# Kernel optimization log

Measured on AMD Instinct MI355X. Metric: run time of the kernel, lower is better.

## Reference

```python
import jax, jax.numpy as jnp
import numpy as np

B, T, E, D, OUT = 2048, 64, 256, 256, 2


def setup_inputs() -> dict:
    key = jax.random.key(0)
    ks = jax.random.split(key, 16)
    s = 0.05
    return {
        "input_encoded": jax.random.normal(ks[0], (B, T, E), dtype=jnp.float32),
        "y_history": jax.random.normal(ks[1], (B, T), dtype=jnp.float32),
        # attn_layer: Linear(2D+E -> E), Tanh, Linear(E -> 1)
        "W1": jax.random.normal(ks[2], (E, 2 * D + E), dtype=jnp.float32) * s,
        "b1": jax.random.normal(ks[3], (E,), dtype=jnp.float32) * s,
        "w2": jax.random.normal(ks[4], (E,), dtype=jnp.float32) * s,
        "b2": jax.random.normal(ks[5], (1,), dtype=jnp.float32) * s,
        # single-layer LSTM(input=OUT, hidden=D); gate order i,f,g,o
        "W_ih": jax.random.normal(ks[6], (4 * D, OUT), dtype=jnp.float32) * s,
        "b_ih": jax.random.normal(ks[7], (4 * D,), dtype=jnp.float32) * s,
        "W_hh": jax.random.normal(ks[8], (4 * D, D), dtype=jnp.float32) * s,
        "b_hh": jax.random.normal(ks[9], (4 * D,), dtype=jnp.float32) * s,
        # fc: Linear(E+T -> OUT) (torch init normal_() std=1; scaled here for stability)
        "W_fc": jax.random.normal(ks[10], (OUT, E + T), dtype=jnp.float32) * s,
        "b_fc": jax.random.normal(ks[11], (OUT,), dtype=jnp.float32) * s,
        # fc_final: Linear(D+E -> OUT)
        "W_final": jax.random.normal(ks[12], (OUT, D + E), dtype=jnp.float32) * s,
        "b_final": jax.random.normal(ks[13], (OUT,), dtype=jnp.float32) * s,
    }


def reference(input_encoded, y_history, W1, b1, w2, b2, W_ih, b_ih, W_hh, b_hh,
              W_fc, b_fc, W_final, b_final):
    Bs, Ts, Es = input_encoded.shape
    Ds = W_hh.shape[1]

    def step(carry, _):
        h, c, _ctx = carry  # h, c: [B, D]
        hc = jnp.concatenate([h, c], axis=-1)  # [B, 2D]
        hc_rep = jnp.broadcast_to(hc[:, None, :], (Bs, Ts, 2 * Ds))
        x = jnp.concatenate([hc_rep, input_encoded], axis=-1)  # [B, T, 2D+E]
        scores = jnp.tanh(x @ W1.T + b1) @ w2 + b2  # [B, T]
        alpha = jax.nn.softmax(scores, axis=1)
        ctx = jnp.einsum('bt,bte->be', alpha, input_encoded)  # [B, E]
        y_tilde = jnp.concatenate([ctx, y_history], axis=1) @ W_fc.T + b_fc  # [B, OUT]
        gates = y_tilde @ W_ih.T + b_ih + h @ W_hh.T + b_hh  # [B, 4D]
        i, f, g, o = jnp.split(gates, 4, axis=-1)
        c_new = jax.nn.sigmoid(f) * c + jax.nn.sigmoid(i) * jnp.tanh(g)
        h_new = jax.nn.sigmoid(o) * jnp.tanh(c_new)
        return (h_new, c_new, ctx), None

    init = (jnp.zeros((Bs, Ds), input_encoded.dtype),
            jnp.zeros((Bs, Ds), input_encoded.dtype),
            jnp.zeros((Bs, Es), input_encoded.dtype))
    (h, c, ctx), _ = jax.lax.scan(step, init, None, length=Ts)
    return jnp.concatenate([h, ctx], axis=1) @ W_final.T + b_final  # [B, OUT]
```

## Files before the change

kernel.cpp:

```cpp
#include <hip/hip_runtime.h>
#include <hip/hip_bf16.h>
#include <cstdint>
#include <cstddef>

#define LOG2E 1.44269504088896340736f

using f32x4 = __attribute__((ext_vector_type(4))) float;
using s16x8 = __attribute__((ext_vector_type(8))) short;

static __device__ __forceinline__ float bf2f(unsigned short u) {
  union { unsigned int i; float f; } v; v.i = ((unsigned int)u) << 16; return v.f;
}
static __device__ __forceinline__ unsigned short f2bf(float f) {
  union { float f; unsigned int i; } v; v.f = f;
  unsigned int r = v.i + 0x7fffu + ((v.i >> 16) & 1u);
  return (unsigned short)(r >> 16);
}
static __device__ __forceinline__ float wredmax(float v) {
  #pragma unroll
  for (int m = 32; m > 0; m >>= 1) v = fmaxf(v, __shfl_xor(v, m, 64));
  return v;
}
static __device__ __forceinline__ float wredsum(float v) {
  #pragma unroll
  for (int m = 32; m > 0; m >>= 1) v += __shfl_xor(v, m, 64);
  return v;
}

__global__ void ktrans(const float* __restrict__ W1, const float* __restrict__ b1,
                       const float* __restrict__ Wih_in, const float* __restrict__ bih,
                       const float* __restrict__ Whh, const float* __restrict__ bhh,
                       const float* __restrict__ Wfc, const float* __restrict__ bfc,
                       const float* __restrict__ yhist,
                       unsigned short* __restrict__ WB1, unsigned short* __restrict__ WBhh,
                       unsigned short* __restrict__ WB1e, float* __restrict__ b1s,
                       float* __restrict__ Wihs, float* __restrict__ gbias,
                       float* __restrict__ yh2)
{
  int idx = blockIdx.x * 256 + threadIdx.x;
  const float TS = 2.f * LOG2E;
  if (idx < 131072) {
    int k = idx >> 8, e = idx & 255;
    WB1[((k >> 3) * 256 + e) * 8 + (k & 7)] = f2bf(TS * W1[e * 768 + k]);
    return;
  }
  idx -= 131072;
  if (idx < 262144) {
    int k = idx >> 10, j = idx & 1023;
    float sc = ((j >> 8) == 2) ? TS : -LOG2E;
    WBhh[((k >> 3) * 1024 + j) * 8 + (k & 7)] = f2bf(sc * Whh[j * 256 + k]);
    return;
  }
  idx -= 262144;
  if (idx < 65536) {
    int k = idx >> 8, e = idx & 255;
    WB1e[((k >> 3) * 256 + e) * 8 + (k & 7)] = f2bf(TS * W1[e * 768 + 512 + k]);
    return;
  }
  idx -= 65536;
  if (idx < 256) { b1s[idx] = TS * b1[idx]; return; }
  idx -= 256;
  if (idx < 2048) {
    int j = idx >> 1;
    float sc = ((j >> 8) == 2) ? TS : -LOG2E;
    Wihs[idx] = sc * Wih_in[idx];
    return;
  }
  idx -= 2048;
  if (idx < 1024) {
    int j = idx;
    float sc = ((j >> 8) == 2) ? TS : -LOG2E;
    gbias[j] = sc * (bih[j] + bhh[j]);
    return;
  }
  idx -= 1024;
  if (idx < 4096) {
    int bq = idx >> 1, o = idx & 1;
    float a = bfc[o];
    for (int t = 0; t < 64; ++t) a = fmaf(yhist[bq * 64 + t], Wfc[o * 320 + 256 + t], a);
    yh2[idx] = a;
    return;
  }
}

__global__ __launch_bounds__(256, 4) void kpre(
    const float* __restrict__ x, const unsigned short* __restrict__ WB1e,
    const float* __restrict__ Wfc,
    unsigned short* __restrict__ P, float* __restrict__ ey)
{
  __shared__ __align__(16) unsigned short xs[16384];
  const int bq = blockIdx.x;
  const int tid = threadIdx.x;
  const int w = tid >> 6, lane = tid & 63;
  const float* __restrict__ xb = x + (size_t)bq * 16384;

  #pragma unroll 4
  for (int it = 0; it < 16; ++it) {
    int idx = it * 256 + tid;
    float4 v = *(const float4*)(xb + (size_t)idx * 4);
    int t = idx >> 6, e0 = (idx & 63) * 4;
    unsigned long long pk = (unsigned long long)f2bf(v.x)
        | ((unsigned long long)f2bf(v.y) << 16)
        | ((unsigned long long)f2bf(v.z) << 32)
        | ((unsigned long long)f2bf(v.w) << 48);
    int ba = (t * 512 + e0 * 2) ^ ((t & 7) << 4);
    *(unsigned long long*)((char*)xs + ba) = pk;
  }
  __syncthreads();

  const int mt = w;
  const int fgrp = lane >> 4, fcol = lane & 15;
  const int trow = mt * 16 + fcol;
  s16x8 af[8];
  #pragma unroll
  for (int kb = 0; kb < 8; ++kb) {
    int e = kb * 32 + fgrp * 8;
    int ba = (trow * 512 + e * 2) ^ ((trow & 7) << 4);
    af[kb] = *(const s16x8*)((char*)xs + ba);
  }
  __syncthreads();

  unsigned short* __restrict__ Pst = xs;
  #pragma unroll
  for (int nt = 0; nt < 16; ++nt) {
    s16x8 bfr[8];
    #pragma unroll
    for (int kb = 0; kb < 8; ++kb)
      bfr[kb] = *(const s16x8*)&WB1e[(size_t)((kb * 4 + fgrp) * 256 + nt * 16 + fcol) * 8];
    f32x4 acc = {0.f, 0.f, 0.f, 0.f};
    #pragma unroll
    for (int kb = 0; kb < 8; ++kb)
      acc = __builtin_amdgcn_mfma_f32_16x16x32_bf16(af[kb], bfr[kb], acc, 0, 0, 0);
    const int ep = nt * 16 + fcol;
    #pragma unroll
    for (int r = 0; r < 4; ++r)
      Pst[(mt * 16 + fgrp * 4 + r) * 256 + ep] = f2bf(acc[r]);
  }
  __syncthreads();

  unsigned int* __restrict__ Pd = (unsigned int*)(P + (size_t)bq * 16384);
  #pragma unroll 4
  for (int d = tid; d < 8192; d += 256) {
    int f = d * 2;
    int ec = f >> 9, t = (f >> 3) & 63, i0 = f & 7;
    unsigned int lo = Pst[t * 256 + ec * 8 + i0];
    unsigned int hi = Pst[t * 256 + ec * 8 + i0 + 1];
    Pd[d] = lo | (hi << 16);
  }

  if (tid < 128) {
    int t = tid >> 1, o = tid & 1;
    float a = 0.f;
    const float* __restrict__ xr = xb + t * 256;
    const float* __restrict__ wr = Wfc + o * 320;
    #pragma unroll 4
    for (int e = 0; e < 256; ++e) a = fmaf(xr[e], wr[e], a);
    ey[((size_t)bq * 64 + t) * 2 + o] = a;
  }
}

#define SIG(X) __builtin_amdgcn_rcpf(1.f + __builtin_amdgcn_exp2f(X))

#define SCCHUNK(PV, EC) do { \
  const float4 qa_ = *(const float4*)(qrow + (EC) * 8); \
  const float4 qc_ = *(const float4*)(qrow + (EC) * 8 + 4); \
  const float4 wa_ = *(const float4*)(w2f + (EC) * 8); \
  const float4 wc_ = *(const float4*)(w2f + (EC) * 8 + 4); \
  a0 = fmaf(wa_.x, SIG(bf2f((unsigned short)(PV)[0]) + qa_.x), a0); \
  a1 = fmaf(wa_.y, SIG(bf2f((unsigned short)(PV)[1]) + qa_.y), a1); \
  a2 = fmaf(wa_.z, SIG(bf2f((unsigned short)(PV)[2]) + qa_.z), a2); \
  a3 = fmaf(wa_.w, SIG(bf2f((unsigned short)(PV)[3]) + qa_.w), a3); \
  a0 = fmaf(wc_.x, SIG(bf2f((unsigned short)(PV)[4]) + qc_.x), a0); \
  a1 = fmaf(wc_.y, SIG(bf2f((unsigned short)(PV)[5]) + qc_.y), a1); \
  a2 = fmaf(wc_.z, SIG(bf2f((unsigned short)(PV)[6]) + qc_.z), a2); \
  a3 = fmaf(wc_.w, SIG(bf2f((unsigned short)(PV)[7]) + qc_.w), a3); \
} while (0)

#define SCL(EC) do { \
  const s16x8 pvL_ = *(const s16x8*)&Plds[b][(EC) - 16][lane][0]; \
  SCCHUNK(pvL_, EC); \
} while (0)

#define AH(KB) (*(const s16x8*)&hcA[(((KB) * 4 + fgrp) * 8 + frow) * 8])

#define GUNIT(U, S0, S1, S2, S3) do { \
  const size_t jb_ = (size_t)((((U) & 3) * 256 + ((U) >> 2) * 128 + w * 16 + fcol)) * 8; \
  const s16x8 wb0_ = *(const s16x8*)&WBhh[jb_ + (size_t)(0 * 4 + fgrp) * 8192]; \
  const s16x8 wb1_ = *(const s16x8*)&WBhh[jb_ + (size_t)(1 * 4 + fgrp) * 8192]; \
  const s16x8 wb2_ = *(const s16x8*)&WBhh[jb_ + (size_t)(2 * 4 + fgrp) * 8192]; \
  const s16x8 wb3_ = *(const s16x8*)&WBhh[jb_ + (size_t)(3 * 4 + fgrp) * 8192]; \
  const s16x8 wb4_ = *(const s16x8*)&WBhh[jb_ + (size_t)(4 * 4 + fgrp) * 8192]; \
  const s16x8 wb5_ = *(const s16x8*)&WBhh[jb_ + (size_t)(5 * 4 + fgrp) * 8192]; \
  const s16x8 wb6_ = *(const s16x8*)&WBhh[jb_ + (size_t)(6 * 4 + fgrp) * 8192]; \
  const s16x8 wb7_ = *(const s16x8*)&WBhh[jb_ + (size_t)(7 * 4 + fgrp) * 8192]; \
  G##U = (f32x4){gb_##U, gb_##U, gb_##U, gb_##U}; \
  S0; S1; S2; S3; \
  G##U = __builtin_amdgcn_mfma_f32_16x16x32_bf16(AH(0), wb0_, G##U, 0, 0, 0); \
  G##U = __builtin_amdgcn_mfma_f32_16x16x32_bf16(AH(1), wb1_, G##U, 0, 0, 0); \
  G##U = __builtin_amdgcn_mfma_f32_16x16x32_bf16(AH(2), wb2_, G##U, 0, 0, 0); \
  G##U = __builtin_amdgcn_mfma_f32_16x16x32_bf16(AH(3), wb3_, G##U, 0, 0, 0); \
  G##U = __builtin_amdgcn_mfma_f32_16x16x32_bf16(AH(4), wb4_, G##U, 0, 0, 0); \
  G##U = __builtin_amdgcn_mfma_f32_16x16x32_bf16(AH(5), wb5_, G##U, 0, 0, 0); \
  G##U = __builtin_amdgcn_mfma_f32_16x16x32_bf16(AH(6), wb6_, G##U, 0, 0, 0); \
  G##U = __builtin_amdgcn_mfma_f32_16x16x32_bf16(AH(7), wb7_, G##U, 0, 0, 0); \
} while (0)

#define PW(CG, R, CV, Gi, Gf, Gg, Go, w0i, w1i, w0f, w1f, w0g, w1g, w0o, w1o) do { \
  const int row_ = (drow0 + (R)) & 7; \
  const int jj_ = (CG) * 128 + w * 16 + fcol; \
  const float y0_ = yt[row_][0], y1_ = yt[row_][1]; \
  const float gi_ = (Gi)[R] + fmaf(w0i, y0_, (w1i) * y1_); \
  const float gf_ = (Gf)[R] + fmaf(w0f, y0_, (w1f) * y1_); \
  const float gg_ = (Gg)[R] + fmaf(w0g, y0_, (w1g) * y1_); \
  const float go_ = (Go)[R] + fmaf(w0o, y0_, (w1o) * y1_); \
  const float si_ = SIG(gi_); \
  const float sf_ = SIG(gf_); \
  const float tg_ = 1.f - 2.f * SIG(gg_); \
  const float so_ = SIG(go_); \
  const float cn_ = sf_ * (CV) + si_ * tg_; \
  (CV) = cn_; \
  const float th_ = 1.f - 2.f * SIG(2.f * LOG2E * cn_); \
  const float hn_ = so_ * th_; \
  if (lane < 32) { \
    hcA[((jj_ >> 3) * 8 + row_) * 8 + (jj_ & 7)] = f2bf(hn_); \
    hcA[((32 + (jj_ >> 3)) * 8 + row_) * 8 + (jj_ & 7)] = f2bf(cn_); \
    if (s == 63) qf[row_][jj_] = hn_; \
  } \
} while (0)

#define PLOADR(U) const s16x8 p##U = *(const s16x8*)(Pb + (size_t)((U) * 64 + lane) * 8);

#define WIGB(U) \
  const int j##U = (((U) & 3) * 256 + ((U) >> 2) * 128 + w * 16 + fcol); \
  const float wi0_##U = Wihs[2 * j##U]; \
  const float wi1_##U = Wihs[2 * j##U + 1]; \
  const float gb_##U = gbias[j##U];

__global__
__attribute__((amdgpu_flat_work_group_size(512, 512), amdgpu_waves_per_eu(1, 2)))
void krecur(
    const float* __restrict__ x, const float* __restrict__ w2g,
    const unsigned short* __restrict__ WB1, const unsigned short* __restrict__ WBhh,
    const float* __restrict__ Wihs, const float* __restrict__ gbias,
    const float* __restrict__ b1s, const float* __restrict__ yh2,
    const float* __restrict__ ey, const unsigned short* __restrict__ P,
    const float* __restrict__ Wfin, const float* __restrict__ bfin,
    float* __restrict__ out)
{
  __shared__ __align__(16) unsigned short Plds[8][16][64][8];
  __shared__ __align__(16) unsigned short hcA[4096];
  __shared__ __align__(16) float qf[8][256];
  __shared__ __align__(16) float w2f[256];
  __shared__ __align__(16) float scAl[8][64];
  __shared__ float yt[8][2];

  const int tid = threadIdx.x;
  const int w = tid >> 6, lane = tid & 63;
  const int b = w;
  const int gbase = blockIdx.x * 8;
  const int gb = gbase + b;

  for (int i = tid; i < 4096; i += 512) hcA[i] = 0;
  if (tid < 256) w2f[tid] = w2g[tid];
  for (int i = tid; i < 8192; i += 512) {
    int row = i >> 10, rem = i & 1023, ec = rem >> 6, t = rem & 63;
    *(s16x8*)&Plds[row][ec][t][0] =
        *(const s16x8*)(P + (size_t)(gbase + row) * 16384 + (size_t)((16 + ec) * 64 + t) * 8);
  }

  const int frow = lane & 7;
  const int fgrp = lane >> 4;
  const int fcol = lane & 15;
  const int drow0 = fgrp * 4;

  const unsigned short* __restrict__ Pb = P + (size_t)gb * 16384;
  PLOADR(0)  PLOADR(1)  PLOADR(2)  PLOADR(3)
  PLOADR(4)  PLOADR(5)  PLOADR(6)  PLOADR(7)
  PLOADR(8)  PLOADR(9)  PLOADR(10) PLOADR(11)
  PLOADR(12) PLOADR(13) PLOADR(14) PLOADR(15)

  const float2 eyv = *(const float2*)(ey + ((size_t)gb * 64 + lane) * 2);
  const float yh0 = yh2[gb * 2], yh1 = yh2[gb * 2 + 1];
  const float b1r0 = b1s[(w * 2 + 0) * 16 + fcol];
  const float b1r1 = b1s[(w * 2 + 1) * 16 + fcol];

  WIGB(0) WIGB(1) WIGB(2) WIGB(3) WIGB(4) WIGB(5) WIGB(6) WIGB(7)

  float c0 = 0.f, c1 = 0.f, c2 = 0.f, c3 = 0.f;
  float c4 = 0.f, c5 = 0.f, c6 = 0.f, c7 = 0.f;

  __syncthreads();

  for (int s = 0; s < 64; ++s) {
    #pragma unroll
    for (int et2 = 0; et2 < 2; ++et2) {
      const int eb = (w * 2 + et2) * 16;
      f32x4 acc = {0.f, 0.f, 0.f, 0.f};
      #pragma unroll
      for (int kb = 0; kb < 16; ++kb) {
        const s16x8 bfr = *(const s16x8*)&WB1[(size_t)((kb * 4 + fgrp) * 256 + eb + fcol) * 8];
        acc = __builtin_amdgcn_mfma_f32_16x16x32_bf16(AH(kb), bfr, acc, 0, 0, 0);
      }
      if (lane < 32) {
        const float bb = et2 ? b1r1 : b1r0;
        #pragma unroll
        for (int r = 0; r < 4; ++r) qf[drow0 + r][eb + fcol] = acc[r] + bb;
      }
    }
    __syncthreads();

    float a0 = 0.f, a1 = 0.f, a2 = 0.f, a3 = 0.f;
    f32x4 G0, G1, G2, G3, G4, G5, G6, G7;
    const float* __restrict__ qrow = &qf[b][0];
    GUNIT(0, SCCHUNK(p0, 0),  SCCHUNK(p1, 1),  SCCHUNK(p2, 2),  SCCHUNK(p3, 3));
    GUNIT(1, SCCHUNK(p4, 4),  SCCHUNK(p5, 5),  SCCHUNK(p6, 6),  SCCHUNK(p7, 7));
    GUNIT(2, SCCHUNK(p8, 8),  SCCHUNK(p9, 9),  SCCHUNK(p10, 10), SCCHUNK(p11, 11));
    GUNIT(3, SCCHUNK(p12, 12), SCCHUNK(p13, 13), SCCHUNK(p14, 14), SCCHUNK(p15, 15));
    GUNIT(4, SCL(16), SCL(17), SCL(18), SCL(19));
    GUNIT(5, SCL(20), SCL(21), SCL(22), SCL(23));
    GUNIT(6, SCL(24), SCL(25), SCL(26), SCL(27));
    GUNIT(7, SCL(28), SCL(29), SCL(30), SCL(31));

    {
      float sc = -2.f * ((a0 + a1) + (a2 + a3));
      float mx = wredmax(sc);
      float e_t = __builtin_amdgcn_exp2f((sc - mx) * LOG2E);
      float sm = wredsum(e_t);
      float alpha = e_t * __builtin_amdgcn_rcpf(sm);
      if (s == 63) scAl[b][lane] = alpha;
      float y0 = wredsum(alpha * eyv.x);
      float y1 = wredsum(alpha * eyv.y);
      if (lane == 0) { yt[b][0] = y0 + yh0; yt[b][1] = y1 + yh1; }
    }
    __syncthreads();

    PW(0, 0, c0, G0, G1, G2, G3, wi0_0, wi1_0, wi0_1, wi1_1, wi0_2, wi1_2, wi0_3, wi1_3);
    PW(0, 1, c1, G0, G1, G2, G3, wi0_0, wi1_0, wi0_1, wi1_1, wi0_2, wi1_2, wi0_3, wi1_3);
    PW(0, 2, c2, G0, G1, G2, G3, wi0_0, wi1_0, wi0_1, wi1_1, wi0_2, wi1_2, wi0_3, wi1_3);
    PW(0, 3, c3, G0, G1, G2, G3, wi0_0, wi1_0, wi0_1, wi1_1, wi0_2, wi1_2, wi0_3, wi1_3);
    PW(1, 0, c4, G4, G5, G6, G7, wi0_4, wi1_4, wi0_5, wi1_5, wi0_6, wi1_6, wi0_7, wi1_7);
    PW(1, 1, c5, G4, G5, G6, G7, wi0_4, wi1_4, wi0_5, wi1_5, wi0_6, wi1_6, wi0_7, wi1_7);
    PW(1, 2, c6, G4, G5, G6, G7, wi0_4, wi1_4, wi0_5, wi1_5, wi0_6, wi1_6, wi0_7, wi1_7);
    PW(1, 3, c7, G4, G5, G6, G7, wi0_4, wi1_4, wi0_5, wi1_5, wi0_6, wi1_6, wi0_7, wi1_7);
    __syncthreads();

    if (s == 63) {
      float* __restrict__ ctxS = (float*)Plds;
      #pragma unroll
      for (int p = 0; p < 4; ++p) {
        const int e = p * 64 + lane;
        float a = 0.f;
        const float* __restrict__ xr = x + (size_t)gb * 16384 + e;
        #pragma unroll 8
        for (int t = 0; t < 64; ++t) a = fmaf(scAl[b][t], xr[t * 256], a);
        ctxS[b * 256 + e] = a;
      }
      __syncthreads();
    }
  }

  {
    const float* __restrict__ ctxS = (const float*)Plds;
    float o0 = 0.f, o1 = 0.f;
    #pragma unroll
    for (int kk = 0; kk < 8; ++kk) {
      const int k = kk * 64 + lane;
      const float v = (k < 256) ? qf[b][k] : ctxS[b * 256 + (k - 256)];
      o0 = fmaf(v, Wfin[k], o0);
      o1 = fmaf(v, Wfin[512 + k], o1);
    }
    o0 = wredsum(o0);
    o1 = wredsum(o1);
    if (lane == 0) {
      out[gb * 2 + 0] = o0 + bfin[0];
      out[gb * 2 + 1] = o1 + bfin[1];
    }
  }
}

extern "C" void kernel_launch(void* const* d_in, const int* in_sizes, int n_in,
                              void* d_out, int out_size, void* d_ws, size_t ws_size,
                              hipStream_t stream) {
  const float* x    = (const float*)d_in[0];
  const float* yh   = (const float*)d_in[1];
  const float* W1   = (const float*)d_in[2];
  const float* b1   = (const float*)d_in[3];
  const float* w2   = (const float*)d_in[4];
  const float* Wih  = (const float*)d_in[6];
  const float* bih  = (const float*)d_in[7];
  const float* Whh  = (const float*)d_in[8];
  const float* bhh  = (const float*)d_in[9];
  const float* Wfc  = (const float*)d_in[10];
  const float* bfc  = (const float*)d_in[11];
  const float* Wfin = (const float*)d_in[12];
  const float* bfin = (const float*)d_in[13];

  char* ws = (char*)d_ws;
  unsigned short* P    = (unsigned short*)(ws + 0);
  unsigned short* WB1  = (unsigned short*)(ws + 67108864);
  unsigned short* WBhh = (unsigned short*)(ws + 67371008);
  unsigned short* WB1e = (unsigned short*)(ws + 67895296);
  float* b1s   = (float*)(ws + 68026368);
  float* Wihs  = (float*)(ws + 68027392);
  float* gbias = (float*)(ws + 68035584);
  float* yh2   = (float*)(ws + 68039680);
  float* ey    = (float*)(ws + 68056064);

  ktrans<<<1821, 256, 0, stream>>>(W1, b1, Wih, bih, Whh, bhh, Wfc, bfc, yh,
                                   WB1, WBhh, WB1e, b1s, Wihs, gbias, yh2);
  kpre<<<2048, 256, 0, stream>>>(x, WB1e, Wfc, P, ey);
  krecur<<<256, 512, 0, stream>>>(x, w2, WB1, WBhh, Wihs, gbias, b1s, yh2, ey, P,
                                  Wfin, bfin, (float*)d_out);
}
```

Before: 4.068 ms.

## Double recurrence block to 1024 threads, splitting score and gate work per wave

The recurrent kernel now runs 16 waves per block instead of 8. Each batch row's attention score is split across two waves, and each wave handles half of the gate units. The LDS-resident half of the precomputed projection is dropped because every wave now holds its whole half in registers. Input-weight and gate-bias vectors move to shared memory, and an extra barrier plus a partial-score exchange buffer are added each step to combine the two halves. This trades more barrier traffic and tighter register budgets (waves_per_eu 4) for more parallel waves per compute unit and shorter per-wave serial work.

```diff
diff --git a/kernel.cpp b/kernel.cpp
--- a/kernel.cpp
+++ b/kernel.cpp
@@ -161,11 +161,11 @@
 
 #define SIG(X) __builtin_amdgcn_rcpf(1.f + __builtin_amdgcn_exp2f(X))
 
-#define SCCHUNK(PV, EC) do { \
-  const float4 qa_ = *(const float4*)(qrow + (EC) * 8); \
-  const float4 qc_ = *(const float4*)(qrow + (EC) * 8 + 4); \
-  const float4 wa_ = *(const float4*)(w2f + (EC) * 8); \
-  const float4 wc_ = *(const float4*)(w2f + (EC) * 8 + 4); \
+#define SCCHUNK(PV, U) do { \
+  const float4 qa_ = *(const float4*)(qrowh + (U) * 8); \
+  const float4 qc_ = *(const float4*)(qrowh + (U) * 8 + 4); \
+  const float4 wa_ = *(const float4*)(w2h + (U) * 8); \
+  const float4 wc_ = *(const float4*)(w2h + (U) * 8 + 4); \
   a0 = fmaf(wa_.x, SIG(bf2f((unsigned short)(PV)[0]) + qa_.x), a0); \
   a1 = fmaf(wa_.y, SIG(bf2f((unsigned short)(PV)[1]) + qa_.y), a1); \
   a2 = fmaf(wa_.z, SIG(bf2f((unsigned short)(PV)[2]) + qa_.z), a2); \
@@ -176,15 +176,11 @@
   a3 = fmaf(wc_.w, SIG(bf2f((unsigned short)(PV)[7]) + qc_.w), a3); \
 } while (0)
 
-#define SCL(EC) do { \
-  const s16x8 pvL_ = *(const s16x8*)&Plds[b][(EC) - 16][lane][0]; \
-  SCCHUNK(pvL_, EC); \
-} while (0)
-
-#define AH(KB) (*(const s16x8*)&hcA[(((KB) * 4 + fgrp) * 8 + frow) * 8])
-
-#define GUNIT(U, S0, S1, S2, S3) do { \
-  const size_t jb_ = (size_t)((((U) & 3) * 256 + ((U) >> 2) * 128 + w * 16 + fcol)) * 8; \
+#define AHF(KB) (*(const s16x8*)&hcA[(((KB) * 4 + fgrp) * 8 + frow) * 8])
+
+#define GUNIT4(GG) do { \
+  const int jg_ = (GG) * 256 + wv * 16 + fcol; \
+  const size_t jb_ = (size_t)jg_ * 8; \
   const s16x8 wb0_ = *(const s16x8*)&WBhh[jb_ + (size_t)(0 * 4 + fgrp) * 8192]; \
   const s16x8 wb1_ = *(const s16x8*)&WBhh[jb_ + (size_t)(1 * 4 + fgrp) * 8192]; \
   const s16x8 wb2_ = *(const s16x8*)&WBhh[jb_ + (size_t)(2 * 4 + fgrp) * 8192]; \
@@ -193,26 +189,25 @@
   const s16x8 wb5_ = *(const s16x8*)&WBhh[jb_ + (size_t)(5 * 4 + fgrp) * 8192]; \
   const s16x8 wb6_ = *(const s16x8*)&WBhh[jb_ + (size_t)(6 * 4 + fgrp) * 8192]; \
   const s16x8 wb7_ = *(const s16x8*)&WBhh[jb_ + (size_t)(7 * 4 + fgrp) * 8192]; \
-  G##U = (f32x4){gb_##U, gb_##U, gb_##U, gb_##U}; \
-  S0; S1; S2; S3; \
-  G##U = __builtin_amdgcn_mfma_f32_16x16x32_bf16(AH(0), wb0_, G##U, 0, 0, 0); \
-  G##U = __builtin_amdgcn_mfma_f32_16x16x32_bf16(AH(1), wb1_, G##U, 0, 0, 0); \
-  G##U = __builtin_amdgcn_mfma_f32_16x16x32_bf16(AH(2), wb2_, G##U, 0, 0, 0); \
-  G##U = __builtin_amdgcn_mfma_f32_16x16x32_bf16(AH(3), wb3_, G##U, 0, 0, 0); \
-  G##U = __builtin_amdgcn_mfma_f32_16x16x32_bf16(AH(4), wb4_, G##U, 0, 0, 0); \
-  G##U = __builtin_amdgcn_mfma_f32_16x16x32_bf16(AH(5), wb5_, G##U, 0, 0, 0); \
-  G##U = __builtin_amdgcn_mfma_f32_16x16x32_bf16(AH(6), wb6_, G##U, 0, 0, 0); \
-  G##U = __builtin_amdgcn_mfma_f32_16x16x32_bf16(AH(7), wb7_, G##U, 0, 0, 0); \
+  const float gbj_ = gbS[jg_]; \
+  GA##GG = (f32x4){gbj_, gbj_, gbj_, gbj_}; \
+  GA##GG = __builtin_amdgcn_mfma_f32_16x16x32_bf16(AHF(0), wb0_, GA##GG, 0, 0, 0); \
+  GA##GG = __builtin_amdgcn_mfma_f32_16x16x32_bf16(AHF(1), wb1_, GA##GG, 0, 0, 0); \
+  GA##GG = __builtin_amdgcn_mfma_f32_16x16x32_bf16(AHF(2), wb2_, GA##GG, 0, 0, 0); \
+  GA##GG = __builtin_amdgcn_mfma_f32_16x16x32_bf16(AHF(3), wb3_, GA##GG, 0, 0, 0); \
+  GA##GG = __builtin_amdgcn_mfma_f32_16x16x32_bf16(AHF(4), wb4_, GA##GG, 0, 0, 0); \
+  GA##GG = __builtin_amdgcn_mfma_f32_16x16x32_bf16(AHF(5), wb5_, GA##GG, 0, 0, 0); \
+  GA##GG = __builtin_amdgcn_mfma_f32_16x16x32_bf16(AHF(6), wb6_, GA##GG, 0, 0, 0); \
+  GA##GG = __builtin_amdgcn_mfma_f32_16x16x32_bf16(AHF(7), wb7_, GA##GG, 0, 0, 0); \
 } while (0)
 
-#define PW(CG, R, CV, Gi, Gf, Gg, Go, w0i, w1i, w0f, w1f, w0g, w1g, w0o, w1o) do { \
-  const int row_ = (drow0 + (R)) & 7; \
-  const int jj_ = (CG) * 128 + w * 16 + fcol; \
+#define PWR(R, CV) do { \
+  const int row_ = drow0 + (R); \
   const float y0_ = yt[row_][0], y1_ = yt[row_][1]; \
-  const float gi_ = (Gi)[R] + fmaf(w0i, y0_, (w1i) * y1_); \
-  const float gf_ = (Gf)[R] + fmaf(w0f, y0_, (w1f) * y1_); \
-  const float gg_ = (Gg)[R] + fmaf(w0g, y0_, (w1g) * y1_); \
-  const float go_ = (Go)[R] + fmaf(w0o, y0_, (w1o) * y1_); \
+  const float gi_ = GA0[R] + fmaf(wI0, y0_, wI1 * y1_); \
+  const float gf_ = GA1[R] + fmaf(wF0, y0_, wF1 * y1_); \
+  const float gg_ = GA2[R] + fmaf(wG0, y0_, wG1 * y1_); \
+  const float go_ = GA3[R] + fmaf(wO0, y0_, wO1 * y1_); \
   const float si_ = SIG(gi_); \
   const float sf_ = SIG(gf_); \
   const float tg_ = 1.f - 2.f * SIG(gg_); \
@@ -221,23 +216,15 @@
   (CV) = cn_; \
   const float th_ = 1.f - 2.f * SIG(2.f * LOG2E * cn_); \
   const float hn_ = so_ * th_; \
-  if (lane < 32) { \
-    hcA[((jj_ >> 3) * 8 + row_) * 8 + (jj_ & 7)] = f2bf(hn_); \
-    hcA[((32 + (jj_ >> 3)) * 8 + row_) * 8 + (jj_ & 7)] = f2bf(cn_); \
-    if (s == 63) qf[row_][jj_] = hn_; \
-  } \
+  hcA[((jj >> 3) * 8 + row_) * 8 + (jj & 7)] = f2bf(hn_); \
+  hcA[((32 + (jj >> 3)) * 8 + row_) * 8 + (jj & 7)] = f2bf(cn_); \
+  if (s == 63) hF[row_][jj] = hn_; \
 } while (0)
 
-#define PLOADR(U) const s16x8 p##U = *(const s16x8*)(Pb + (size_t)((U) * 64 + lane) * 8);
-
-#define WIGB(U) \
-  const int j##U = (((U) & 3) * 256 + ((U) >> 2) * 128 + w * 16 + fcol); \
-  const float wi0_##U = Wihs[2 * j##U]; \
-  const float wi1_##U = Wihs[2 * j##U + 1]; \
-  const float gb_##U = gbias[j##U];
+#define PLOADR(U) const s16x8 p##U = *(const s16x8*)(Pb + (U) * 512 + lane * 8);
 
 __global__
-__attribute__((amdgpu_flat_work_group_size(512, 512), amdgpu_waves_per_eu(1, 2)))
+__attribute__((amdgpu_flat_work_group_size(1024, 1024), amdgpu_waves_per_eu(4, 4)))
 void krecur(
     const float* __restrict__ x, const float* __restrict__ w2g,
     const unsigned short* __restrict__ WB1, const unsigned short* __restrict__ WBhh,
@@ -247,33 +234,36 @@
     const float* __restrict__ Wfin, const float* __restrict__ bfin,
     float* __restrict__ out)
 {
-  __shared__ __align__(16) unsigned short Plds[8][16][64][8];
   __shared__ __align__(16) unsigned short hcA[4096];
   __shared__ __align__(16) float qf[8][256];
   __shared__ __align__(16) float w2f[256];
+  __shared__ __align__(16) float ps[8][2][64];
   __shared__ __align__(16) float scAl[8][64];
   __shared__ float yt[8][2];
+  __shared__ __align__(16) float wi0S[1024];
+  __shared__ __align__(16) float wi1S[1024];
+  __shared__ __align__(16) float gbS[1024];
+  __shared__ __align__(16) float hF[8][256];
+  __shared__ __align__(16) float ctxS[8][256];
 
   const int tid = threadIdx.x;
-  const int w = tid >> 6, lane = tid & 63;
-  const int b = w;
+  const int wv = tid >> 6, lane = tid & 63;
+  const int row = wv >> 1, half = wv & 1;
   const int gbase = blockIdx.x * 8;
-  const int gb = gbase + b;
-
-  for (int i = tid; i < 4096; i += 512) hcA[i] = 0;
+  const int gb = gbase + row;
+
+  for (int i = tid; i < 4096; i += 1024) hcA[i] = 0;
   if (tid < 256) w2f[tid] = w2g[tid];
-  for (int i = tid; i < 8192; i += 512) {
-    int row = i >> 10, rem = i & 1023, ec = rem >> 6, t = rem & 63;
-    *(s16x8*)&Plds[row][ec][t][0] =
-        *(const s16x8*)(P + (size_t)(gbase + row) * 16384 + (size_t)((16 + ec) * 64 + t) * 8);
-  }
+  wi0S[tid] = Wihs[2 * tid];
+  wi1S[tid] = Wihs[2 * tid + 1];
+  gbS[tid]  = gbias[tid];
 
   const int frow = lane & 7;
   const int fgrp = lane >> 4;
   const int fcol = lane & 15;
   const int drow0 = fgrp * 4;
 
-  const unsigned short* __restrict__ Pb = P + (size_t)gb * 16384;
+  const unsigned short* __restrict__ Pb = P + (size_t)gb * 16384 + (size_t)half * 8192;
   PLOADR(0)  PLOADR(1)  PLOADR(2)  PLOADR(3)
   PLOADR(4)  PLOADR(5)  PLOADR(6)  PLOADR(7)
   PLOADR(8)  PLOADR(9)  PLOADR(10) PLOADR(11)
@@ -281,91 +271,84 @@
 
   const float2 eyv = *(const float2*)(ey + ((size_t)gb * 64 + lane) * 2);
   const float yh0 = yh2[gb * 2], yh1 = yh2[gb * 2 + 1];
-  const float b1r0 = b1s[(w * 2 + 0) * 16 + fcol];
-  const float b1r1 = b1s[(w * 2 + 1) * 16 + fcol];
-
-  WIGB(0) WIGB(1) WIGB(2) WIGB(3) WIGB(4) WIGB(5) WIGB(6) WIGB(7)
+  const float b1r = b1s[wv * 16 + fcol];
 
   float c0 = 0.f, c1 = 0.f, c2 = 0.f, c3 = 0.f;
-  float c4 = 0.f, c5 = 0.f, c6 = 0.f, c7 = 0.f;
 
   __syncthreads();
 
   for (int s = 0; s < 64; ++s) {
-    #pragma unroll
-    for (int et2 = 0; et2 < 2; ++et2) {
-      const int eb = (w * 2 + et2) * 16;
+    {
       f32x4 acc = {0.f, 0.f, 0.f, 0.f};
       #pragma unroll
       for (int kb = 0; kb < 16; ++kb) {
-        const s16x8 bfr = *(const s16x8*)&WB1[(size_t)((kb * 4 + fgrp) * 256 + eb + fcol) * 8];
-        acc = __builtin_amdgcn_mfma_f32_16x16x32_bf16(AH(kb), bfr, acc, 0, 0, 0);
+        const s16x8 bfr = *(const s16x8*)&WB1[(size_t)((kb * 4 + fgrp) * 256 + wv * 16 + fcol) * 8];
+        acc = __builtin_amdgcn_mfma_f32_16x16x32_bf16(AHF(kb), bfr, acc, 0, 0, 0);
       }
       if (lane < 32) {
-        const float bb = et2 ? b1r1 : b1r0;
         #pragma unroll
-        for (int r = 0; r < 4; ++r) qf[drow0 + r][eb + fcol] = acc[r] + bb;
+        for (int r = 0; r < 4; ++r) qf[drow0 + r][wv * 16 + fcol] = acc[r] + b1r;
       }
     }
     __syncthreads();
 
-    float a0 = 0.f, a1 = 0.f, a2 = 0.f, a3 = 0.f;
-    f32x4 G0, G1, G2, G3, G4, G5, G6, G7;
-    const float* __restrict__ qrow = &qf[b][0];
-    GUNIT(0, SCCHUNK(p0, 0),  SCCHUNK(p1, 1),  SCCHUNK(p2, 2),  SCCHUNK(p3, 3));
-    GUNIT(1, SCCHUNK(p4, 4),  SCCHUNK(p5, 5),  SCCHUNK(p6, 6),  SCCHUNK(p7, 7));
-    GUNIT(2, SCCHUNK(p8, 8),  SCCHUNK(p9, 9),  SCCHUNK(p10, 10), SCCHUNK(p11, 11));
-    GUNIT(3, SCCHUNK(p12, 12), SCCHUNK(p13, 13), SCCHUNK(p14, 14), SCCHUNK(p15, 15));
-    GUNIT(4, SCL(16), SCL(17), SCL(18), SCL(19));
-    GUNIT(5, SCL(20), SCL(21), SCL(22), SCL(23));
-    GUNIT(6, SCL(24), SCL(25), SCL(26), SCL(27));
-    GUNIT(7, SCL(28), SCL(29), SCL(30), SCL(31));
-
     {
-      float sc = -2.f * ((a0 + a1) + (a2 + a3));
+      const float* __restrict__ qrowh = &qf[row][0] + half * 128;
+      const float* __restrict__ w2h = w2f + half * 128;
+      float a0 = 0.f, a1 = 0.f, a2 = 0.f, a3 = 0.f;
+      SCCHUNK(p0, 0);   SCCHUNK(p1, 1);   SCCHUNK(p2, 2);   SCCHUNK(p3, 3);
+      SCCHUNK(p4, 4);   SCCHUNK(p5, 5);   SCCHUNK(p6, 6);   SCCHUNK(p7, 7);
+      SCCHUNK(p8, 8);   SCCHUNK(p9, 9);   SCCHUNK(p10, 10); SCCHUNK(p11, 11);
+      SCCHUNK(p12, 12); SCCHUNK(p13, 13); SCCHUNK(p14, 14); SCCHUNK(p15, 15);
+      ps[row][half][lane] = (a0 + a1) + (a2 + a3);
+    }
+    __syncthreads();
+
+    f32x4 GA0, GA1, GA2, GA3;
+    GUNIT4(0); GUNIT4(1); GUNIT4(2); GUNIT4(3);
+    {
+      float sc = -2.f * (ps[row][0][lane] + ps[row][1][lane]);
       float mx = wredmax(sc);
       float e_t = __builtin_amdgcn_exp2f((sc - mx) * LOG2E);
       float sm = wredsum(e_t);
       float alpha = e_t * __builtin_amdgcn_rcpf(sm);
-      if (s == 63) scAl[b][lane] = alpha;
+      if (s == 63 && half == 0) scAl[row][lane] = alpha;
       float y0 = wredsum(alpha * eyv.x);
       float y1 = wredsum(alpha * eyv.y);
-      if (lane == 0) { yt[b][0] = y0 + yh0; yt[b][1] = y1 + yh1; }
+      if (half == 0 && lane == 0) { yt[row][0] = y0 + yh0; yt[row][1] = y1 + yh1; }
     }
     __syncthreads();
 
-    PW(0, 0, c0, G0, G1, G2, G3, wi0_0, wi1_0, wi0_1, wi1_1, wi0_2, wi1_2, wi0_3, wi1_3);
-    PW(0, 1, c1, G0, G1, G2, G3, wi0_0, wi1_0, wi0_1, wi1_1, wi0_2, wi1_2, wi0_3, wi1_3);
-    PW(0, 2, c2, G0, G1, G2, G3, wi0_0, wi1_0, wi0_1, wi1_1, wi0_2, wi1_2, wi0_3, wi1_3);
-    PW(0, 3, c3, G0, G1, G2, G3, wi0_0, wi1_0, wi0_1, wi1_1, wi0_2, wi1_2, wi0_3, wi1_3);
-    PW(1, 0, c4, G4, G5, G6, G7, wi0_4, wi1_4, wi0_5, wi1_5, wi0_6, wi1_6, wi0_7, wi1_7);
-    PW(1, 1, c5, G4, G5, G6, G7, wi0_4, wi1_4, wi0_5, wi1_5, wi0_6, wi1_6, wi0_7, wi1_7);
-    PW(1, 2, c6, G4, G5, G6, G7, wi0_4, wi1_4, wi0_5, wi1_5, wi0_6, wi1_6, wi0_7, wi1_7);
-    PW(1, 3, c7, G4, G5, G6, G7, wi0_4, wi1_4, wi0_5, wi1_5, wi0_6, wi1_6, wi0_7, wi1_7);
+    if (lane < 32) {
+      const int jj = wv * 16 + fcol;
+      const float wI0 = wi0S[jj],       wI1 = wi1S[jj];
+      const float wF0 = wi0S[256 + jj], wF1 = wi1S[256 + jj];
+      const float wG0 = wi0S[512 + jj], wG1 = wi1S[512 + jj];
+      const float wO0 = wi0S[768 + jj], wO1 = wi1S[768 + jj];
+      PWR(0, c0); PWR(1, c1); PWR(2, c2); PWR(3, c3);
+    }
     __syncthreads();
 
     if (s == 63) {
-      float* __restrict__ ctxS = (float*)Plds;
       #pragma unroll
-      for (int p = 0; p < 4; ++p) {
-        const int e = p * 64 + lane;
+      for (int pp = 0; pp < 2; ++pp) {
+        const int e = (half * 2 + pp) * 64 + lane;
         float a = 0.f;
         const float* __restrict__ xr = x + (size_t)gb * 16384 + e;
         #pragma unroll 8
-        for (int t = 0; t < 64; ++t) a = fmaf(scAl[b][t], xr[t * 256], a);
-        ctxS[b * 256 + e] = a;
+        for (int t = 0; t < 64; ++t) a = fmaf(scAl[row][t], xr[t * 256], a);
+        ctxS[row][e] = a;
       }
       __syncthreads();
     }
   }
 
-  {
-    const float* __restrict__ ctxS = (const float*)Plds;
+  if (half == 0) {
     float o0 = 0.f, o1 = 0.f;
     #pragma unroll
     for (int kk = 0; kk < 8; ++kk) {
       const int k = kk * 64 + lane;
-      const float v = (k < 256) ? qf[b][k] : ctxS[b * 256 + (k - 256)];
+      const float v = (k < 256) ? hF[row][k] : ctxS[row][k - 256];
       o0 = fmaf(v, Wfin[k], o0);
       o1 = fmaf(v, Wfin[512 + k], o1);
     }
@@ -409,6 +392,6 @@
   ktrans<<<1821, 256, 0, stream>>>(W1, b1, Wih, bih, Whh, bhh, Wfc, bfc, yh,
                                    WB1, WBhh, WB1e, b1s, Wihs, gbias, yh2);
   kpre<<<2048, 256, 0, stream>>>(x, WB1e, Wfc, P, ey);
-  krecur<<<256, 512, 0, stream>>>(x, w2, WB1, WBhh, Wihs, gbias, b1s, yh2, ey, P,
-                                  Wfin, bfin, (float*)d_out);
-}
+  krecur<<<256, 1024, 0, stream>>>(x, w2, WB1, WBhh, Wihs, gbias, b1s, yh2, ey, P,
+                                   Wfin, bfin, (float*)d_out);
+}
```

After: 4.571 ms. +12.4%, slower.
